# Kernel tuning notes

Measured on AMD Instinct MI355X. Metric: run time of the kernel, lower is better.

Reference implementation:

```python
import jax, jax.numpy as jnp
import numpy as np

B, S, D, H, F = 4, 2048, 1024, 16, 4096
BS = 64               # sparse attention block size
DH = D // H           # head dim
EPS = 1e-5


def _layer_norm(x, g, b):
    m = jnp.mean(x, axis=-1, keepdims=True)
    v = jnp.mean(jnp.square(x - m), axis=-1, keepdims=True)
    return (x - m) * jax.lax.rsqrt(v + EPS) * g + b


def setup_inputs() -> dict:
    key = jax.random.key(0)
    ks = jax.random.split(key, 12)
    sc = 0.02
    return {
        "hidden_states": jax.random.normal(ks[0], (B, S, D), dtype=jnp.float32),
        "ln1_g": jnp.ones((D,), jnp.float32), "ln1_b": jnp.zeros((D,), jnp.float32),
        "ln2_g": jnp.ones((D,), jnp.float32), "ln2_b": jnp.zeros((D,), jnp.float32),
        "wq": jax.random.normal(ks[1], (D, D), jnp.float32) * sc, "bq": jnp.zeros((D,), jnp.float32),
        "wk": jax.random.normal(ks[2], (D, D), jnp.float32) * sc, "bk": jnp.zeros((D,), jnp.float32),
        "wv": jax.random.normal(ks[3], (D, D), jnp.float32) * sc, "bv": jnp.zeros((D,), jnp.float32),
        "wo": jax.random.normal(ks[4], (D, D), jnp.float32) * sc, "bo": jnp.zeros((D,), jnp.float32),
        "w1": jax.random.normal(ks[5], (D, F), jnp.float32) * sc, "b1": jnp.zeros((F,), jnp.float32),
        "w2": jax.random.normal(ks[6], (F, D), jnp.float32) * sc, "b2": jnp.zeros((D,), jnp.float32),
    }


def _heads(x, w, b):
    # [B,S,D] -> [B,H,S/BS,BS,DH] block layout
    y = (x @ w + b).reshape(B, S, H, DH).transpose(0, 2, 1, 3)
    return y.reshape(B, H, S // BS, BS, DH)


def _block_attention(x, wq, bq, wk, bk, wv, bv, wo, bo):
    q = _heads(x, wq, bq)
    k = _heads(x, wk, bk)
    v = _heads(x, wv, bv)
    scores = jnp.einsum("bhnqd,bhnkd->bhnqk", q, k) / jnp.sqrt(jnp.float32(DH))
    w = jax.nn.softmax(scores, axis=-1)           # block-local (sparse) attention weights
    o = jnp.einsum("bhnqk,bhnkd->bhnqd", w, v)
    o = o.reshape(B, H, S, DH).transpose(0, 2, 1, 3).reshape(B, S, D)
    return o @ wo + bo, w


def reference(hidden_states, ln1_g, ln1_b, ln2_g, ln2_b,
              wq, bq, wk, bk, wv, bv, wo, bo, w1, b1, w2, b2):
    # pre-norm attention + residual
    x1 = _layer_norm(hidden_states, ln1_g, ln1_b)
    attn_out, attn_w = _block_attention(x1, wq, bq, wk, bk, wv, bv, wo, bo)
    h = hidden_states + attn_out
    # pre-norm FFN + residual (exact GELU, matching torch nn.GELU default)
    x2 = _layer_norm(h, ln2_g, ln2_b)
    ff = jax.nn.gelu(x2 @ w1 + b1, approximate=False) @ w2 + b2
    return h + ff, attn_w
```

## Files before the change

kernel.cpp:

```cpp
#include <hip/hip_runtime.h>
#include <hip/hip_bf16.h>
#include <cmath>

using bf16 = __hip_bfloat16;
typedef __attribute__((ext_vector_type(8))) short short8;
typedef __attribute__((ext_vector_type(4))) float f32x4;

#define LDK 72

__device__ __forceinline__ float bf2f(bf16 v){ return __bfloat162float(v); }
__device__ __forceinline__ bf16 f2bf(float v){ return __float2bfloat16(v); }

__device__ __forceinline__ void ld16(const void* g, void* l) {
    __builtin_amdgcn_global_load_lds(
        (const __attribute__((address_space(1))) void*)g,
        (__attribute__((address_space(3))) void*)l, 16, 0, 0);
}

__device__ __forceinline__ float gelu_f(float x) {
    float u = 0.7978845608028654f * x * (1.0f + 0.044715f * x * x);
    float e = __expf(2.0f * u);
    float t = 1.0f - 2.0f / (e + 1.0f);
    return 0.5f * x * (1.0f + t);
}

__global__ __launch_bounds__(256) void transpose_f32_bf16(
    const float* __restrict__ in, bf16* __restrict__ out, int R, int C)
{
    __shared__ __align__(16) bf16 tile[64][72];
    const int c0 = blockIdx.x * 64, r0 = blockIdx.y * 64;
    const int t = threadIdx.x;
    const int lr = t >> 3, lc = (t & 7) * 8;
    for (int p = 0; p < 2; ++p) {
        int r = p * 32 + lr;
        const float* src = in + (size_t)(r0 + r) * C + c0 + lc;
        float4 a = *(const float4*)src;
        float4 b = *(const float4*)(src + 4);
        tile[r][lc + 0] = f2bf(a.x); tile[r][lc + 1] = f2bf(a.y);
        tile[r][lc + 2] = f2bf(a.z); tile[r][lc + 3] = f2bf(a.w);
        tile[r][lc + 4] = f2bf(b.x); tile[r][lc + 5] = f2bf(b.y);
        tile[r][lc + 6] = f2bf(b.z); tile[r][lc + 7] = f2bf(b.w);
    }
    __syncthreads();
    for (int p = 0; p < 2; ++p) {
        int r = p * 32 + lr;
        short8 v;
        for (int j = 0; j < 8; ++j) v[j] = *(const short*)&tile[lc + j][r];
        *(short8*)(out + (size_t)(c0 + r) * R + r0 + lc) = v;
    }
}

__global__ __launch_bounds__(256) void concat_bias(
    const float* __restrict__ bq, const float* __restrict__ bk,
    const float* __restrict__ bv, float* __restrict__ out)
{
    int i = blockIdx.x * 256 + threadIdx.x;
    const float* src = (i < 1024) ? bq : ((i < 2048) ? bk : bv);
    out[i] = src[i & 1023];
}

__global__ __launch_bounds__(256) void layernorm_k(
    const float* __restrict__ x, const float* __restrict__ g,
    const float* __restrict__ bta, bf16* __restrict__ out)
{
    const int row = blockIdx.x, t = threadIdx.x;
    const float* xr = x + (size_t)row * 1024;
    float v[4], s1 = 0.f, s2 = 0.f;
    for (int j = 0; j < 4; ++j) {
        float f = xr[j * 256 + t];
        v[j] = f; s1 += f; s2 += f * f;
    }
    for (int d = 1; d < 64; d <<= 1) { s1 += __shfl_xor(s1, d); s2 += __shfl_xor(s2, d); }
    __shared__ float red[2][4];
    int wave = t >> 6, lane = t & 63;
    if (lane == 0) { red[0][wave] = s1; red[1][wave] = s2; }
    __syncthreads();
    s1 = red[0][0] + red[0][1] + red[0][2] + red[0][3];
    s2 = red[1][0] + red[1][1] + red[1][2] + red[1][3];
    float mean = s1 * (1.0f / 1024.0f);
    float var  = s2 * (1.0f / 1024.0f) - mean * mean;
    float rs   = rsqrtf(var + 1e-5f);
    bf16* orow = out + (size_t)row * 1024;
    for (int j = 0; j < 4; ++j) {
        int c = j * 256 + t;
        orow[c] = f2bf((v[j] - mean) * rs * g[c] + bta[c]);
    }
}

template <int MODE, int TM>
__global__ __launch_bounds__(256) void gemm_bt(
    const bf16* __restrict__ A, const bf16* __restrict__ Bt,
    const float* __restrict__ bias, const float* __restrict__ res,
    void* __restrict__ C, int M, int N, int K)
{
    constexpr int MI = TM / 32;
    __shared__ __align__(16) bf16 As[TM * 64];
    __shared__ __align__(16) bf16 Bs[128 * 64];
    const int m0 = blockIdx.x * TM, n0 = blockIdx.y * 128;
    const int t = threadIdx.x;
    const int wave = t >> 6, lane = t & 63, lhi = lane >> 4, llo = lane & 15;
    const int wm = (wave & 1) * (TM / 2), wn = (wave >> 1) * 64;
    const int lrow = lane >> 3;
    const int lcolsw = ((lane & 7) ^ lrow) * 8;

    const bf16* Ag = A  + (size_t)(m0 + lrow) * K + lcolsw;
    const bf16* Bg = Bt + (size_t)(n0 + lrow) * K + lcolsw;

    f32x4 acc[MI][4];
    for (int i = 0; i < MI; ++i)
        for (int j = 0; j < 4; ++j) acc[i][j] = (f32x4){0.f, 0.f, 0.f, 0.f};

    auto issue = [&](int k0) {
        for (int p = 0; p < TM / 32; ++p) {
            int rb = wave * (TM / 4) + p * 8;
            ld16(Ag + (size_t)rb * K + k0, &As[rb * 64]);
        }
        for (int p = 0; p < 4; ++p) {
            int rb = wave * 32 + p * 8;
            ld16(Bg + (size_t)rb * K + k0, &Bs[rb * 64]);
        }
    };
    auto compute = [&]() {
        for (int kk = 0; kk < 64; kk += 32) {
            const int gb = kk >> 3;
            short8 af[MI], bfr[4];
            for (int i = 0; i < MI; ++i) {
                int row = wm + i * 16 + llo;
                af[i] = *(const short8*)&As[row * 64 + (((gb + lhi) ^ (llo & 7)) * 8)];
            }
            for (int i = 0; i < 4; ++i) {
                int row = wn + i * 16 + llo;
                bfr[i] = *(const short8*)&Bs[row * 64 + (((gb + lhi) ^ (llo & 7)) * 8)];
            }
            for (int mi = 0; mi < MI; ++mi)
                for (int ni = 0; ni < 4; ++ni)
                    acc[mi][ni] = __builtin_amdgcn_mfma_f32_16x16x32_bf16(
                        af[mi], bfr[ni], acc[mi][ni], 0, 0, 0);
        }
    };

    issue(0);
    __syncthreads();
    for (int k0 = 0; ; ) {
        compute();
        k0 += 64;
        if (k0 >= K) break;
        __syncthreads();
        issue(k0);
        __syncthreads();
    }

    for (int mi = 0; mi < MI; ++mi)
        for (int ni = 0; ni < 4; ++ni) {
            int row = m0 + wm + mi * 16 + lhi * 4;
            int col = n0 + wn + ni * 16 + llo;
            float bcol = bias[col];
            for (int r = 0; r < 4; ++r) {
                size_t idx = (size_t)(row + r) * N + col;
                float v = acc[mi][ni][r] + bcol;
                if (MODE == 0) {
                    ((bf16*)C)[idx] = f2bf(v);
                } else if (MODE == 1) {
                    ((float*)C)[idx] = v + res[idx];
                } else if (MODE == 2) {
                    ((bf16*)C)[idx] = f2bf(gelu_f(v));
                } else {
                    ((float*)C)[idx] = v + res[idx];
                }
            }
        }
}

__global__ __launch_bounds__(256) void attn_kernel(
    const bf16* __restrict__ qkv, float* __restrict__ attw, bf16* __restrict__ o)
{
    __shared__ __align__(16) bf16 qs[64][LDK];
    __shared__ __align__(16) bf16 ks[64][LDK];
    __shared__ __align__(16) bf16 vs[64][LDK];
    const int gid = blockIdx.x;
    const int blk = gid & 31, h = (gid >> 5) & 15, b = gid >> 9;
    const int t = threadIdx.x, wave = t >> 6, lane = t & 63;
    const int lhi = lane >> 4, llo = lane & 15;
    const int srow = t >> 3, scol = (t & 7) * 8;

    for (int p = 0; p < 2; ++p) {
        int r = p * 32 + srow;
        const bf16* base = qkv + (size_t)(b * 2048 + blk * 64 + r) * 3072 + h * 64 + scol;
        *(short8*)&qs[r][scol] = *(const short8*)(base);
        *(short8*)&ks[r][scol] = *(const short8*)(base + 1024);
        *(short8*)&vs[r][scol] = *(const short8*)(base + 2048);
    }
    __syncthreads();

    f32x4 sacc[4];
    for (int j = 0; j < 4; ++j) sacc[j] = (f32x4){0.f, 0.f, 0.f, 0.f};
    for (int kk = 0; kk < 64; kk += 32) {
        short8 aq = *(const short8*)&qs[wave * 16 + llo][kk + lhi * 8];
        for (int j = 0; j < 4; ++j) {
            short8 bk = *(const short8*)&ks[j * 16 + llo][kk + lhi * 8];
            sacc[j] = __builtin_amdgcn_mfma_f32_16x16x32_bf16(aq, bk, sacc[j], 0, 0, 0);
        }
    }
    float inv[4];
    for (int r = 0; r < 4; ++r) {
        float m = -1e30f;
        for (int j = 0; j < 4; ++j) m = fmaxf(m, sacc[j][r]);
        for (int d = 1; d < 16; d <<= 1) m = fmaxf(m, __shfl_xor(m, d));
        float s = 0.f;
        for (int j = 0; j < 4; ++j) {
            float e = expf((sacc[j][r] - m) * 0.125f);
            sacc[j][r] = e; s += e;
        }
        for (int d = 1; d < 16; d <<= 1) s += __shfl_xor(s, d);
        inv[r] = 1.0f / s;
    }
    __syncthreads();
    const size_t wbase = (size_t)gid * 4096;
    for (int j = 0; j < 4; ++j)
        for (int r = 0; r < 4; ++r) {
            int row = wave * 16 + lhi * 4 + r, col = j * 16 + llo;
            float pw = sacc[j][r] * inv[r];
            qs[row][col] = f2bf(pw);
            attw[wbase + row * 64 + col] = pw;
        }
    __syncthreads();

    f32x4 oacc[4];
    for (int nt = 0; nt < 4; ++nt) oacc[nt] = (f32x4){0.f, 0.f, 0.f, 0.f};
    for (int kk = 0; kk < 64; kk += 32) {
        short8 aw = *(const short8*)&qs[wave * 16 + llo][kk + lhi * 8];
        for (int nt = 0; nt < 4; ++nt) {
            short8 bv;
            for (int jj = 0; jj < 8; ++jj)
                bv[jj] = *(const short*)&vs[kk + lhi * 8 + jj][nt * 16 + llo];
            oacc[nt] = __builtin_amdgcn_mfma_f32_16x16x32_bf16(aw, bv, oacc[nt], 0, 0, 0);
        }
    }
    for (int nt = 0; nt < 4; ++nt)
        for (int r = 0; r < 4; ++r) {
            int row = wave * 16 + lhi * 4 + r, col = nt * 16 + llo;
            o[(size_t)(b * 2048 + blk * 64 + row) * 1024 + h * 64 + col] = f2bf(oacc[nt][r]);
        }
}

extern "C" void kernel_launch(void* const* d_in, const int* in_sizes, int n_in,
                              void* d_out, int out_size, void* d_ws, size_t ws_size,
                              hipStream_t stream)
{
    const float* hidden = (const float*)d_in[0];
    const float* ln1_g  = (const float*)d_in[1];
    const float* ln1_b  = (const float*)d_in[2];
    const float* ln2_g  = (const float*)d_in[3];
    const float* ln2_b  = (const float*)d_in[4];
    const float* wq = (const float*)d_in[5];  const float* bq = (const float*)d_in[6];
    const float* wk = (const float*)d_in[7];  const float* bk = (const float*)d_in[8];
    const float* wv = (const float*)d_in[9];  const float* bv = (const float*)d_in[10];
    const float* wo = (const float*)d_in[11]; const float* bo = (const float*)d_in[12];
    const float* w1 = (const float*)d_in[13]; const float* b1 = (const float*)d_in[14];
    const float* w2 = (const float*)d_in[15]; const float* b2 = (const float*)d_in[16];

    char* ws = (char*)d_ws;
    const size_t MB = 1u << 20;
    bf16*  wqkvT   = (bf16*)(ws +  0 * MB);
    bf16*  woT     = (bf16*)(ws +  6 * MB);
    bf16*  w1T     = (bf16*)(ws +  8 * MB);
    bf16*  w2T     = (bf16*)(ws + 16 * MB);
    float* biasQKV = (float*)(ws + 24 * MB);
    bf16*  x       = (bf16*)(ws + 25 * MB);
    bf16*  qkv     = (bf16*)(ws + 41 * MB);
    float* hbuf    = (float*)(ws + 41 * MB);
    bf16*  ffc     = (bf16*)(ws + 73 * MB);
    bf16*  obuf    = (bf16*)(ws + 89 * MB);

    float* out0 = (float*)d_out;
    float* attw = (float*)d_out + (size_t)8192 * 1024;

    transpose_f32_bf16<<<dim3(16, 16), 256, 0, stream>>>(wq, wqkvT,                 1024, 1024);
    transpose_f32_bf16<<<dim3(16, 16), 256, 0, stream>>>(wk, wqkvT + 1024 * 1024,   1024, 1024);
    transpose_f32_bf16<<<dim3(16, 16), 256, 0, stream>>>(wv, wqkvT + 2*1024*1024,   1024, 1024);
    transpose_f32_bf16<<<dim3(16, 16), 256, 0, stream>>>(wo, woT, 1024, 1024);
    transpose_f32_bf16<<<dim3(64, 16), 256, 0, stream>>>(w1, w1T, 1024, 4096);
    transpose_f32_bf16<<<dim3(16, 64), 256, 0, stream>>>(w2, w2T, 4096, 1024);
    concat_bias<<<12, 256, 0, stream>>>(bq, bk, bv, biasQKV);

    layernorm_k<<<8192, 256, 0, stream>>>(hidden, ln1_g, ln1_b, x);

    gemm_bt<0, 128><<<dim3(64, 24), 256, 0, stream>>>(x, wqkvT, biasQKV, nullptr, qkv,
                                                      8192, 3072, 1024);

    attn_kernel<<<2048, 256, 0, stream>>>(qkv, attw, obuf);

    gemm_bt<1, 64><<<dim3(128, 8), 256, 0, stream>>>(obuf, woT, bo, hidden, hbuf,
                                                     8192, 1024, 1024);

    layernorm_k<<<8192, 256, 0, stream>>>(hbuf, ln2_g, ln2_b, x);

    gemm_bt<2, 128><<<dim3(64, 32), 256, 0, stream>>>(x, w1T, b1, nullptr, ffc,
                                                      8192, 4096, 1024);

    gemm_bt<3, 64><<<dim3(128, 8), 256, 0, stream>>>(ffc, w2T, b2, hbuf, out0,
                                                     8192, 1024, 4096);
}
```

Before: 447.4 us.

## Add 256x256-tile double-buffered GEMM for QKV and FFN1, widen other GEMM tiles

Adds a new 512-thread GEMM kernel with 256x256 output tiles, a K-step of 32, double-buffered LDS staging through direct global-to-LDS loads, swizzled LDS reads and explicit waitcnt/barrier scheduling. It is used for the QKV projection and the first FFN GEMM (with GELU fused). The output-projection and FFN2 GEMMs switch from 64-row to 128-row tiles. Larger tiles raise data reuse per byte loaded, but they leave fewer blocks per GPU (384 and 512) and put more register pressure on the 128-accumulator kernel.

Measured after the change: 449.1 us. Within noise of the previous version (+0.4%).

```diff
diff --git a/kernel.cpp b/kernel.cpp
--- a/kernel.cpp
+++ b/kernel.cpp
@@ -85,6 +85,103 @@
         int c = j * 256 + t;
         orow[c] = f2bf((v[j] - mean) * rs * g[c] + bta[c]);
     }
+}
+
+template <int MODE>
+__global__ __launch_bounds__(512, 2) void gemm256(
+    const bf16* __restrict__ A, const bf16* __restrict__ Bt,
+    const float* __restrict__ bias, void* __restrict__ C,
+    int M, int N, int K)
+{
+    __shared__ __align__(16) bf16 smem[2][2][256 * 32];
+    const int m0 = blockIdx.x * 256, n0 = blockIdx.y * 256;
+    const int t = threadIdx.x;
+    const int wave = t >> 6, lane = t & 63, lhi = lane >> 4, llo = lane & 15;
+    const int wm = (wave >> 2) * 128;
+    const int wn = (wave & 3) * 64;
+
+    const int r_st = wave * 16 + (lane >> 2);
+    const int gsw  = (lane & 3) ^ ((r_st >> 1) & 3);
+    const bf16* Abase = A  + (size_t)(m0 + r_st) * K + gsw * 8;
+    const bf16* Bbase = Bt + (size_t)(n0 + r_st) * K + gsw * 8;
+
+    auto stageA = [&](int j, int b) {
+        const bf16* s = Abase + j * 32;
+        ld16(s,                   &smem[b][0][wave * 512]);
+        ld16(s + (size_t)128 * K, &smem[b][0][(8 + wave) * 512]);
+    };
+    auto stageB = [&](int j, int b) {
+        const bf16* s = Bbase + j * 32;
+        ld16(s,                   &smem[b][1][wave * 512]);
+        ld16(s + (size_t)128 * K, &smem[b][1][(8 + wave) * 512]);
+    };
+    const int grd = (llo >> 1) & 3;
+    auto rdA = [&](int b, int mi) {
+        return *(const short8*)&smem[b][0][(wm + mi * 16 + llo) * 32 + ((lhi ^ grd) * 8)];
+    };
+    auto rdB = [&](int b, int ni) {
+        return *(const short8*)&smem[b][1][(wn + ni * 16 + llo) * 32 + ((lhi ^ grd) * 8)];
+    };
+
+    f32x4 acc[8][4];
+    #pragma unroll
+    for (int i = 0; i < 8; ++i)
+        #pragma unroll
+        for (int j = 0; j < 4; ++j) acc[i][j] = (f32x4){0.f, 0.f, 0.f, 0.f};
+
+    const int T = K >> 5;
+    stageA(0, 0); stageB(0, 0);
+
+    for (int j = 0; j < T; ++j) {
+        const int cb = j & 1;
+        if (j + 1 < T) {
+            stageA(j + 1, cb ^ 1);
+            stageB(j + 1, cb ^ 1);
+            asm volatile("s_waitcnt vmcnt(4)" ::: "memory");
+        } else {
+            asm volatile("s_waitcnt vmcnt(0)" ::: "memory");
+        }
+        __builtin_amdgcn_sched_barrier(0);
+        __builtin_amdgcn_s_barrier();
+        __builtin_amdgcn_sched_barrier(0);
+
+        short8 af[8], bfr[4];
+        #pragma unroll
+        for (int mi = 0; mi < 8; ++mi) af[mi] = rdA(cb, mi);
+        #pragma unroll
+        for (int ni = 0; ni < 4; ++ni) bfr[ni] = rdB(cb, ni);
+        __builtin_amdgcn_s_setprio(1);
+        #pragma unroll
+        for (int mi = 0; mi < 8; ++mi)
+            #pragma unroll
+            for (int ni = 0; ni < 4; ++ni)
+                acc[mi][ni] = __builtin_amdgcn_mfma_f32_16x16x32_bf16(
+                    af[mi], bfr[ni], acc[mi][ni], 0, 0, 0);
+        __builtin_amdgcn_s_setprio(0);
+
+        if (j + 1 < T) {
+            asm volatile("s_waitcnt lgkmcnt(0)" ::: "memory");
+            __builtin_amdgcn_sched_barrier(0);
+            __builtin_amdgcn_s_barrier();
+            __builtin_amdgcn_sched_barrier(0);
+        }
+    }
+
+    #pragma unroll
+    for (int mi = 0; mi < 8; ++mi)
+        #pragma unroll
+        for (int ni = 0; ni < 4; ++ni) {
+            int row = m0 + wm + mi * 16 + lhi * 4;
+            int col = n0 + wn + ni * 16 + llo;
+            float bcol = bias[col];
+            #pragma unroll
+            for (int r = 0; r < 4; ++r) {
+                size_t idx = (size_t)(row + r) * N + col;
+                float v = acc[mi][ni][r] + bcol;
+                if (MODE == 2) ((bf16*)C)[idx] = f2bf(gelu_f(v));
+                else           ((bf16*)C)[idx] = f2bf(v);
+            }
+        }
 }
 
 template <int MODE, int TM>
@@ -285,19 +382,19 @@
 
     layernorm_k<<<8192, 256, 0, stream>>>(hidden, ln1_g, ln1_b, x);
 
-    gemm_bt<0, 128><<<dim3(64, 24), 256, 0, stream>>>(x, wqkvT, biasQKV, nullptr, qkv,
-                                                      8192, 3072, 1024);
+    gemm256<0><<<dim3(32, 12), 512, 0, stream>>>(x, wqkvT, biasQKV, qkv,
+                                                 8192, 3072, 1024);
 
     attn_kernel<<<2048, 256, 0, stream>>>(qkv, attw, obuf);
 
-    gemm_bt<1, 64><<<dim3(128, 8), 256, 0, stream>>>(obuf, woT, bo, hidden, hbuf,
+    gemm_bt<1, 128><<<dim3(64, 8), 256, 0, stream>>>(obuf, woT, bo, hidden, hbuf,
                                                      8192, 1024, 1024);
 
     layernorm_k<<<8192, 256, 0, stream>>>(hbuf, ln2_g, ln2_b, x);
 
-    gemm_bt<2, 128><<<dim3(64, 32), 256, 0, stream>>>(x, w1T, b1, nullptr, ffc,
-                                                      8192, 4096, 1024);
-
-    gemm_bt<3, 64><<<dim3(128, 8), 256, 0, stream>>>(ffc, w2T, b2, hbuf, out0,
+    gemm256<2><<<dim3(32, 16), 512, 0, stream>>>(x, w1T, b1, ffc,
+                                                 8192, 4096, 1024);
+
+    gemm_bt<3, 128><<<dim3(64, 8), 256, 0, stream>>>(ffc, w2T, b2, hbuf, out0,
                                                      8192, 1024, 4096);
 }
```
